# Performance work log

Measured on AMD Instinct MI355X. Metric: run time of the kernel, lower is better.

The kernel has to match this reference:

```python
import jax, jax.numpy as jnp
import numpy as np

N_PTS0 = 32   # sample points per line
N_PTS1 = 8    # after maxpool1d (kernel/stride = 4)
DIM_LOI = 128
DIM_FC = 1024
TOPK = 300
HW = 128
NLINES = 20000
NLAB = 3


def setup_inputs() -> dict:
    key = jax.random.key(0)
    ks = jax.random.split(key, 10)
    jloc = jax.random.uniform(ks[0], (1, HW, HW), dtype=jnp.float32)
    joff = jax.random.uniform(ks[1], (2, HW, HW), dtype=jnp.float32)
    loi_features = jax.random.normal(ks[2], (DIM_LOI, HW, HW), dtype=jnp.float32)
    edge_idx = jax.random.randint(ks[3], (NLINES, 2), 0, TOPK, dtype=jnp.int32)
    W1 = jax.random.normal(ks[4], (DIM_LOI * N_PTS1, DIM_FC), dtype=jnp.float32) * 0.02
    b1 = jnp.zeros((DIM_FC,), jnp.float32)
    W2 = jax.random.normal(ks[5], (DIM_FC, DIM_FC), dtype=jnp.float32) * 0.02
    b2 = jnp.zeros((DIM_FC,), jnp.float32)
    W3 = jax.random.normal(ks[6], (DIM_FC, NLAB), dtype=jnp.float32) * 0.02
    b3 = jnp.zeros((NLAB,), jnp.float32)
    return {"jloc": jloc, "joff": joff, "loi_features": loi_features,
            "edge_idx": edge_idx, "W1": W1, "b1": b1, "W2": W2, "b2": b2,
            "W3": W3, "b3": b3}


def reference(jloc, joff, loi_features, edge_idx, W1, b1, W2, b2, W3, b3):
    C, h, w = loi_features.shape
    # --- NMS: 3x3 max_pool2d, keep only local maxima ---
    ap = jax.lax.reduce_window(jloc, -jnp.inf, jax.lax.max,
                               (1, 3, 3), (1, 1, 1), 'SAME')
    jloc_nms = jloc * (jloc == ap).astype(jloc.dtype)
    # --- top-k junction decoding (joff_pred = sigmoid(joff) - 0.5) ---
    joff_pred = jax.nn.sigmoid(joff) - 0.5
    scores, idx = jax.lax.top_k(jloc_nms.reshape(-1), TOPK)
    joff_flat = joff_pred.reshape(2, -1)
    y = (idx // w).astype(jnp.float32) + joff_flat[1][idx] + 0.5
    x = (idx % w).astype(jnp.float32) + joff_flat[0][idx] + 0.5
    juncs = jnp.stack((x, y), axis=1)                       # [K, 2]
    # --- lines from junction pairs (lines_adjusted) ---
    lines = jnp.concatenate((juncs[edge_idx[:, 0]], juncs[edge_idx[:, 1]]), axis=1)  # [N, 4]
    # --- LOI pooling: bilinear sampling along each line ---
    tspan = jnp.linspace(0.0, 1.0, N_PTS0)                  # [P]
    U, V = lines[:, :2], lines[:, 2:]
    pts = U[:, :, None] * tspan + V[:, :, None] * (1.0 - tspan) - 0.5  # [N, 2, P]
    pts = pts.transpose(0, 2, 1).reshape(-1, 2)             # [N*P, 2]
    px, py = pts[:, 0], pts[:, 1]
    px0 = jnp.clip(jnp.floor(px), 0, w - 1)
    py0 = jnp.clip(jnp.floor(py), 0, h - 1)
    px1 = jnp.clip(px0 + 1, 0, w - 1)
    py1 = jnp.clip(py0 + 1, 0, h - 1)
    px0l, py0l = px0.astype(jnp.int32), py0.astype(jnp.int32)
    px1l, py1l = px1.astype(jnp.int32), py1.astype(jnp.int32)
    xp = (loi_features[:, py0l, px0l] * (py1 - py) * (px1 - px)
          + loi_features[:, py1l, px0l] * (py - py0) * (px1 - px)
          + loi_features[:, py0l, px1l] * (py1 - py) * (px - px0)
          + loi_features[:, py1l, px1l] * (py - py0) * (px - px0))  # [C, N*P]
    xp = xp.reshape(C, -1, N_PTS0).transpose(1, 0, 2)        # [N, C, P]
    k = N_PTS0 // N_PTS1
    xp = xp.reshape(xp.shape[0], C, N_PTS1, k).max(axis=-1)  # maxpool1d
    feats = xp.reshape(xp.shape[0], C * N_PTS1)              # [N, C*n_pts1]
    # --- fc2 MLP head ---
    h1 = jax.nn.relu(feats @ W1 + b1)
    h2 = jax.nn.relu(h1 @ W2 + b2)
    line_logits = h2 @ W3 + b3
    return line_logits
```

## Files before the change

### kernel.cpp

```cpp
#include <hip/hip_runtime.h>
#include <cmath>


typedef _Float16 f16;
typedef _Float16 f16x2 __attribute__((ext_vector_type(2)));
typedef _Float16 f16x8 __attribute__((ext_vector_type(8)));
typedef float f32x4 __attribute__((ext_vector_type(4)));

#define HWD 128
#define NPIX 16384
#define TOPK_N 300
#define NLINES 20000
#define MPAD 20160
#define KDIM 1024
#define NDIM 1024
#define MAXCAND 4096


#define G2L(gp, lp) __builtin_amdgcn_global_load_lds( \
    (const __attribute__((address_space(1))) void*)(gp), \
    (__attribute__((address_space(3))) void*)(lp), 16, 0, 0)

__global__ __launch_bounds__(256) void preproc_kernel(
    const float* __restrict__ loi, f16* __restrict__ loiT,
    const float* __restrict__ W1, f16* __restrict__ W1T,
    const float* __restrict__ W2, f16* __restrict__ W2T,
    const float* __restrict__ jloc, unsigned long long* __restrict__ cand,
    int* __restrict__ count, float* __restrict__ out, int out_n)
{
    const int bid = blockIdx.x;
    const int tid = threadIdx.x;
    if (bid < 128) {
        __shared__ f16 t[128 * 130];
        const int y = bid;
        #pragma unroll 4
        for (int it = 0; it < 64; ++it) {
            int idx = it * 256 + tid;
            int c = idx >> 7, x = idx & 127;
            t[x * 130 + c] = (f16)loi[c * NPIX + y * HWD + x];
        }
        __syncthreads();
        #pragma unroll
        for (int it = 0; it < 8; ++it) {
            int j = it * 256 + tid;
            int x = j >> 4, cc = (j & 15) * 8;
            f16x8 v;
            #pragma unroll
            for (int u = 0; u < 8; ++u) v[u] = t[x * 130 + cc + u];
            *(f16x8*)(loiT + (y * HWD + x) * HWD + cc) = v;
        }
    } else if (bid < 640) {
        const int b = bid - 128;
        const float* W = (b < 256) ? W1 : W2;
        f16* Wt = (b < 256) ? W1T : W2T;
        const int bb = b & 255;
        __shared__ f16 t[64 * 66];
        const int k0 = (bb >> 4) * 64;
        const int n0 = (bb & 15) * 64;
        #pragma unroll 4
        for (int it = 0; it < 16; ++it) {
            int i = it * 256 + tid;
            int r = i >> 6, c = i & 63;
            t[c * 66 + r] = (f16)W[(size_t)(k0 + r) * NDIM + n0 + c];
        }
        __syncthreads();
        #pragma unroll
        for (int it = 0; it < 2; ++it) {
            int j = it * 256 + tid;
            int nr = j >> 3, kc = (j & 7) * 8;
            f16x8 v;
            #pragma unroll
            for (int u = 0; u < 8; ++u) v[u] = t[nr * 66 + kc + u];
            const int kk = k0 + kc;
            const int n = n0 + nr;
            const int slot = ((kk >> 3) & 3) ^ ((n >> 1) & 3);
            *(f16x8*)(Wt + ((size_t)(kk >> 5) * NDIM + n) * 32 + slot * 8) = v;
        }
    } else if (bid < 704) {
        const int p = (bid - 640) * 256 + tid;
        const int y = p >> 7, x = p & 127;
        const float c = jloc[p];
        float m = c;
        for (int dy = -1; dy <= 1; ++dy) {
            int yy = y + dy;
            if (yy < 0 || yy >= HWD) continue;
            for (int dx = -1; dx <= 1; ++dx) {
                int xx = x + dx;
                if (xx < 0 || xx >= HWD) continue;
                m = fmaxf(m, jloc[yy * HWD + xx]);
            }
        }
        if (c == m && c > 0.0f) {
            int pos = atomicAdd(count, 1);
            if (pos < MAXCAND) {
                unsigned int ub = __float_as_uint(c);
                cand[pos] = ((unsigned long long)ub << 32) |
                            (unsigned long long)(0xFFFFFFFFu - (unsigned int)p);
            }
        }
    } else {
        const int base = (bid - 704) * 1024 + tid * 4;
        #pragma unroll
        for (int u = 0; u < 4; ++u)
            if (base + u < out_n) out[base + u] = 0.f;
    }
}

__global__ __launch_bounds__(256) void rank_junc_kernel(
    const unsigned long long* __restrict__ cand, const int* __restrict__ count,
    const float* __restrict__ joff, float* __restrict__ juncs )
{
    __shared__ unsigned long long keys[MAXCAND];
    const int n = min(*count, MAXCAND);
    const int t = blockIdx.x * 256 + threadIdx.x;
    for (int i = threadIdx.x; i < n; i += 256)
        keys[i] = cand[i];
    __syncthreads();
    if (t >= n) return;
    const unsigned long long key = keys[t];
    int rank = 0;
    int j = 0;
    for (; j + 4 <= n; j += 4) {
        rank += (keys[j]     > key);
        rank += (keys[j + 1] > key);
        rank += (keys[j + 2] > key);
        rank += (keys[j + 3] > key);
    }
    for (; j < n; ++j) rank += (keys[j] > key);
    if (rank < TOPK_N) {
        unsigned int p = 0xFFFFFFFFu - (unsigned int)(key & 0xFFFFFFFFull);
        float sx = 1.0f / (1.0f + expf(-joff[p]));
        float sy = 1.0f / (1.0f + expf(-joff[NPIX + p]));
        juncs[2 * rank + 0] = (float)(p & 127) + sx;
        juncs[2 * rank + 1] = (float)(p >> 7) + sy;
    }
}

__global__ __launch_bounds__(256) void sample_kernel(
    const f16* __restrict__ loiT, const float* __restrict__ juncs,
    const int* __restrict__ edge_idx, f16* __restrict__ feats)
{
    const int wv = threadIdx.x >> 6;
    const int l = blockIdx.x * 4 + wv;
    const int lane = threadIdx.x & 63;

    __shared__ int   soff[4][32][4];
    __shared__ float swt[4][32][4];

    if (lane < 32) {
        const int e0 = edge_idx[2 * l], e1 = edge_idx[2 * l + 1];
        const float ux = juncs[2 * e0], uy = juncs[2 * e0 + 1];
        const float vx = juncs[2 * e1], vy = juncs[2 * e1 + 1];
        const int j = lane;
        const float t = (float)j * (1.0f / 31.0f);
        const float px = ux * t + vx * (1.0f - t) - 0.5f;
        const float py = uy * t + vy * (1.0f - t) - 0.5f;
        float fx0 = fminf(fmaxf(floorf(px), 0.0f), 127.0f);
        float fy0 = fminf(fmaxf(floorf(py), 0.0f), 127.0f);
        float fx1 = fminf(fx0 + 1.0f, 127.0f);
        float fy1 = fminf(fy0 + 1.0f, 127.0f);
        int ix0 = (int)fx0, iy0 = (int)fy0, ix1 = (int)fx1, iy1 = (int)fy1;
        soff[wv][j][0] = (iy0 * HWD + ix0) * HWD;
        soff[wv][j][1] = (iy1 * HWD + ix0) * HWD;
        soff[wv][j][2] = (iy0 * HWD + ix1) * HWD;
        soff[wv][j][3] = (iy1 * HWD + ix1) * HWD;
        swt[wv][j][0] = (fy1 - py) * (fx1 - px);
        swt[wv][j][1] = (py - fy0) * (fx1 - px);
        swt[wv][j][2] = (fy1 - py) * (px - fx0);
        swt[wv][j][3] = (py - fy0) * (px - fx0);
    }
    __syncthreads();

    const int c2 = lane * 2;
    f16x8 o0, o1;
    #pragma unroll
    for (int p = 0; p < 8; ++p) {
        float m0 = -INFINITY, m1 = -INFINITY;
        #pragma unroll
        for (int jj = 0; jj < 4; ++jj) {
            const int j = p * 4 + jj;
            const int b00 = soff[wv][j][0], b10 = soff[wv][j][1];
            const int b01 = soff[wv][j][2], b11 = soff[wv][j][3];
            const float w00 = swt[wv][j][0], w10 = swt[wv][j][1];
            const float w01 = swt[wv][j][2], w11 = swt[wv][j][3];
            f16x2 v00 = *(const f16x2*)(loiT + b00 + c2);
            f16x2 v10 = *(const f16x2*)(loiT + b10 + c2);
            f16x2 v01 = *(const f16x2*)(loiT + b01 + c2);
            f16x2 v11 = *(const f16x2*)(loiT + b11 + c2);
            float s0 = (float)v00.x * w00 + (float)v10.x * w10 +
                       (float)v01.x * w01 + (float)v11.x * w11;
            float s1 = (float)v00.y * w00 + (float)v10.y * w10 +
                       (float)v01.y * w01 + (float)v11.y * w11;
            m0 = fmaxf(m0, s0);
            m1 = fmaxf(m1, s1);
        }
        o0[p] = (f16)m0;
        o1[p] = (f16)m1;
    }
    const int rs = (l >> 1) & 3;
    const int oct0 = (lane & 1) * 2;
    f16* base = feats + ((size_t)(lane >> 1) * MPAD + l) * 32;
    *(f16x8*)(base + ((oct0 ^ rs) * 8)) = o0;
    *(f16x8*)(base + (((oct0 + 1) ^ rs) * 8)) = o1;
}

__global__ __launch_bounds__(256, 2) void gemm_bias_relu_kernel(
    const f16* __restrict__ A, const f16* __restrict__ Bt,
    const float* __restrict__ bias, f16* __restrict__ C,
    const float* __restrict__ W3, const float* __restrict__ b3,
    float* __restrict__ out, int K, int head)
{
    extern __shared__ f16 lds[];
    const int tid = threadIdx.x;
    const int wave = tid >> 6, lane = tid & 63;
    const int wm = wave >> 1, wn = wave & 1;
    const int m0 = blockIdx.y * 160;
    const int n0 = blockIdx.x * 256;

    const int col16 = lane & 15;
    const int quad = lane >> 4;
    const int swz = (quad ^ ((col16 >> 1) & 3)) * 8;

    f32x4 acc[5][8];
    #pragma unroll
    for (int mi = 0; mi < 5; ++mi)
        #pragma unroll
        for (int ni = 0; ni < 8; ++ni)
            acc[mi][ni] = (f32x4){0.f, 0.f, 0.f, 0.f};

    const size_t strideA = (size_t)MPAD * 32;
    const size_t strideB = (size_t)NDIM * 32;
    const f16* gA = A + (size_t)m0 * 32 + wave * 512 + lane * 8;
    const f16* gB = Bt + (size_t)n0 * 32 + wave * 2048 + lane * 8;
    const int sAo = wave * 512;
    const int sBo = wave * 2048;

#define STAGE(CN) do { \
        f16* lb_ = lds + ((CN) % 3) * 13312; \
        const f16* ga_ = gA + (size_t)(CN) * strideA; \
        G2L(ga_,        lb_ + sAo); \
        G2L(ga_ + 2048, lb_ + sAo + 2048); \
        if (wave < 2) G2L(ga_ + 4096, lb_ + sAo + 4096); \
        const f16* gb_ = gB + (size_t)(CN) * strideB; \
        G2L(gb_,        lb_ + 5120 + sBo); \
        G2L(gb_ + 512,  lb_ + 5120 + sBo + 512); \
        G2L(gb_ + 1024, lb_ + 5120 + sBo + 1024); \
        G2L(gb_ + 1536, lb_ + 5120 + sBo + 1536); \
    } while (0)

    STAGE(0);
    asm volatile("" ::: "memory");
    STAGE(1);
    asm volatile("" ::: "memory");

    const int NC = K >> 5;
    for (int c = 0; c < NC; ++c) {
        if (c + 1 < NC) {
            if (wave < 2) asm volatile("s_waitcnt vmcnt(7)" ::: "memory");
            else          asm volatile("s_waitcnt vmcnt(6)" ::: "memory");
        } else {
            asm volatile("s_waitcnt vmcnt(0)" ::: "memory");
        }
        __builtin_amdgcn_s_barrier();
        if (c + 2 < NC) STAGE(c + 2);
        asm volatile("" ::: "memory");

        const f16* buf = lds + (c % 3) * 13312;
        const f16* pA = buf + (wm * 80 + col16) * 32 + swz;
        const f16* pB = buf + 5120 + (wn * 128 + col16) * 32 + swz;
        f16x8 af[5], bf[8];
        #pragma unroll
        for (int i = 0; i < 5; ++i)
            af[i] = *(const f16x8*)(pA + i * 512);
        #pragma unroll
        for (int i = 0; i < 8; ++i)
            bf[i] = *(const f16x8*)(pB + i * 512);
        #pragma unroll
        for (int mi = 0; mi < 5; ++mi)
            #pragma unroll
            for (int ni = 0; ni < 8; ++ni)
                acc[mi][ni] = __builtin_amdgcn_mfma_f32_16x16x32_f16(
                    af[mi], bf[ni], acc[mi][ni], 0, 0, 0);
    }
#undef STAGE

    if (!head) {
        #pragma unroll
        for (int ni = 0; ni < 8; ++ni) {
            const int n = n0 + wn * 128 + ni * 16 + col16;
            const float b = bias[n];
            const size_t rb = (size_t)(n >> 5) * MPAD;
            const int noct = (n >> 3) & 3, ne = n & 7;
            #pragma unroll
            for (int mi = 0; mi < 5; ++mi) {
                #pragma unroll
                for (int r = 0; r < 4; ++r) {
                    const int m = m0 + wm * 80 + mi * 16 + quad * 4 + r;
                    float v = fmaxf(acc[mi][ni][r] + b, 0.f);
                    C[(rb + m) * 32 + ((noct ^ ((m >> 1) & 3)) * 8) + ne] = (f16)v;
                }
            }
        }
    } else {
        float bb[8], w3c[8][3];
        #pragma unroll
        for (int ni = 0; ni < 8; ++ni) {
            const int n = n0 + wn * 128 + ni * 16 + col16;
            bb[ni] = bias[n];
            #pragma unroll
            for (int jj = 0; jj < 3; ++jj) w3c[ni][jj] = W3[n * 3 + jj];
        }
        const bool addb3 = (blockIdx.x == 0 && wn == 0);
        #pragma unroll
        for (int mi = 0; mi < 5; ++mi) {
            #pragma unroll
            for (int r = 0; r < 4; ++r) {
                float s0 = 0.f, s1 = 0.f, s2 = 0.f;
                #pragma unroll
                for (int ni = 0; ni < 8; ++ni) {
                    float v = fmaxf(acc[mi][ni][r] + bb[ni], 0.f);
                    s0 += v * w3c[ni][0];
                    s1 += v * w3c[ni][1];
                    s2 += v * w3c[ni][2];
                }
                #pragma unroll
                for (int mask = 1; mask <= 8; mask <<= 1) {
                    s0 += __shfl_xor(s0, mask);
                    s1 += __shfl_xor(s1, mask);
                    s2 += __shfl_xor(s2, mask);
                }
                if (col16 == 0) {
                    const int m = m0 + wm * 80 + mi * 16 + quad * 4 + r;
                    if (m < NLINES) {
                        atomicAdd(&out[m * 3 + 0], s0 + (addb3 ? b3[0] : 0.f));
                        atomicAdd(&out[m * 3 + 1], s1 + (addb3 ? b3[1] : 0.f));
                        atomicAdd(&out[m * 3 + 2], s2 + (addb3 ? b3[2] : 0.f));
                    }
                }
            }
        }
    }
}

extern "C" void kernel_launch(void* const* d_in, const int* in_sizes, int n_in,
                              void* d_out, int out_size, void* d_ws, size_t ws_size,
                              hipStream_t stream)
{
    const float* jloc = (const float*)d_in[0];
    const float* joff = (const float*)d_in[1];
    const float* loi  = (const float*)d_in[2];
    const int*   eidx = (const int*)d_in[3];
    const float* W1   = (const float*)d_in[4];
    const float* b1   = (const float*)d_in[5];
    const float* W2   = (const float*)d_in[6];
    const float* b2   = (const float*)d_in[7];
    const float* W3   = (const float*)d_in[8];
    const float* b3   = (const float*)d_in[9];
    float* out = (float*)d_out;

    char* ws = (char*)d_ws;
    f16*   loiT  = (f16*)(ws);
    f16*   W1T   = (f16*)(ws + ((size_t)4 << 20));
    f16*   W2T   = (f16*)(ws + ((size_t)6 << 20));
    float* juncs = (float*)(ws + ((size_t)8 << 20));
    int*   count = (int*)(ws + ((size_t)8 << 20) + 4096);
    unsigned long long* cand =
        (unsigned long long*)(ws + ((size_t)8 << 20) + 8192);
    f16*   feats = (f16*)(ws + ((size_t)9 << 20));
    f16*   h1    = (f16*)(ws + ((size_t)52 << 20));

    static int attr_done = 0;
    if (!attr_done) {
        (void)hipFuncSetAttribute(
            reinterpret_cast<const void*>(&gemm_bias_relu_kernel),
            hipFuncAttributeMaxDynamicSharedMemorySize, 79872);
        attr_done = 1;
    }

    hipMemsetAsync(count, 0, sizeof(int), stream);
    preproc_kernel<<<dim3(764), dim3(256), 0, stream>>>(
        loi, loiT, W1, W1T, W2, W2T, jloc, cand, count, out, out_size);
    rank_junc_kernel<<<dim3(MAXCAND / 256), dim3(256), 0, stream>>>(
        cand, count, joff, juncs);
    sample_kernel<<<dim3(NLINES / 4), dim3(256), 0, stream>>>(loiT, juncs, eidx, feats);
    gemm_bias_relu_kernel<<<dim3(NDIM / 256, MPAD / 160), dim3(256), 79872, stream>>>(
        feats, W1T, b1, h1, nullptr, nullptr, nullptr, KDIM, 0);
    gemm_bias_relu_kernel<<<dim3(NDIM / 256, MPAD / 160), dim3(256), 79872, stream>>>(
        h1, W2T, b2, nullptr, W3, b3, out, KDIM, 1);
}
```

Measured before the change: 277.8 us.

## Double GEMM K-step per stage to 64 with larger LDS ring buffers

Each pipeline stage of the GEMM now loads two 32-wide K chunks per barrier, so each LDS buffer holds 64 of K and the triple-buffered ring grows to about 156 KB. The aim is to halve the number of barriers and waitcnt synchronisation points and keep more loads in flight. In exchange, occupancy drops to one block per CU (launch bounds changed from 2 to 1), so there is less latency hiding across blocks.

```diff
diff --git a/kernel.cpp b/kernel.cpp
--- a/kernel.cpp
+++ b/kernel.cpp
@@ -204,7 +204,7 @@
     *(f16x8*)(base + (((oct0 + 1) ^ rs) * 8)) = o1;
 }
 
-__global__ __launch_bounds__(256, 2) void gemm_bias_relu_kernel(
+__global__ __launch_bounds__(256, 1) void gemm_bias_relu_kernel(
     const f16* __restrict__ A, const f16* __restrict__ Bt,
     const float* __restrict__ bias, f16* __restrict__ C,
     const float* __restrict__ W3, const float* __restrict__ b3,
@@ -230,22 +230,26 @@
 
     const size_t strideA = (size_t)MPAD * 32;
     const size_t strideB = (size_t)NDIM * 32;
-    const f16* gA = A + (size_t)m0 * 32 + wave * 512 + lane * 8;
-    const f16* gB = Bt + (size_t)n0 * 32 + wave * 2048 + lane * 8;
-    const int sAo = wave * 512;
-    const int sBo = wave * 2048;
-
-#define STAGE(CN) do { \
-        f16* lb_ = lds + ((CN) % 3) * 13312; \
-        const f16* ga_ = gA + (size_t)(CN) * strideA; \
-        G2L(ga_,        lb_ + sAo); \
-        G2L(ga_ + 2048, lb_ + sAo + 2048); \
-        if (wave < 2) G2L(ga_ + 4096, lb_ + sAo + 4096); \
-        const f16* gb_ = gB + (size_t)(CN) * strideB; \
-        G2L(gb_,        lb_ + 5120 + sBo); \
-        G2L(gb_ + 512,  lb_ + 5120 + sBo + 512); \
-        G2L(gb_ + 1024, lb_ + 5120 + sBo + 1024); \
-        G2L(gb_ + 1536, lb_ + 5120 + sBo + 1536); \
+    const f16* gA = A + (size_t)m0 * 32 + lane * 8;
+    const f16* gB = Bt + (size_t)n0 * 32 + lane * 8;
+
+#define STAGE(R) do { \
+        f16* lb_ = lds + ((R) % 3) * 26624; \
+        const f16* gar_ = gA + (size_t)(2 * (R)) * strideA; \
+        _Pragma("unroll") \
+        for (int i_ = 0; i_ < 5; ++i_) { \
+            const int s_ = wave + 4 * i_; \
+            const f16* g_ = gar_ + (s_ >= 10 ? strideA : 0) + (s_ % 10) * 512; \
+            G2L(g_, lb_ + s_ * 512); \
+        } \
+        const f16* gbr_ = gB + (size_t)(2 * (R)) * strideB \
+                          + (wave >= 2 ? strideB : 0); \
+        const int sb0_ = 8 * wave; \
+        _Pragma("unroll") \
+        for (int j_ = 0; j_ < 8; ++j_) { \
+            const int sB_ = sb0_ + j_; \
+            G2L(gbr_ + (sB_ & 15) * 512, lb_ + 10240 + sB_ * 512); \
+        } \
     } while (0)
 
     STAGE(0);
@@ -253,34 +257,51 @@
     STAGE(1);
     asm volatile("" ::: "memory");
 
-    const int NC = K >> 5;
-    for (int c = 0; c < NC; ++c) {
-        if (c + 1 < NC) {
-            if (wave < 2) asm volatile("s_waitcnt vmcnt(7)" ::: "memory");
-            else          asm volatile("s_waitcnt vmcnt(6)" ::: "memory");
-        } else {
+    const int NR = K >> 6;
+    for (int r = 0; r < NR; ++r) {
+        if (r + 1 < NR)
+            asm volatile("s_waitcnt vmcnt(13)" ::: "memory");
+        else
             asm volatile("s_waitcnt vmcnt(0)" ::: "memory");
-        }
         __builtin_amdgcn_s_barrier();
-        if (c + 2 < NC) STAGE(c + 2);
+        if (r + 2 < NR) STAGE(r + 2);
         asm volatile("" ::: "memory");
 
-        const f16* buf = lds + (c % 3) * 13312;
-        const f16* pA = buf + (wm * 80 + col16) * 32 + swz;
-        const f16* pB = buf + 5120 + (wn * 128 + col16) * 32 + swz;
-        f16x8 af[5], bf[8];
-        #pragma unroll
-        for (int i = 0; i < 5; ++i)
-            af[i] = *(const f16x8*)(pA + i * 512);
-        #pragma unroll
-        for (int i = 0; i < 8; ++i)
-            bf[i] = *(const f16x8*)(pB + i * 512);
-        #pragma unroll
-        for (int mi = 0; mi < 5; ++mi)
-            #pragma unroll
-            for (int ni = 0; ni < 8; ++ni)
-                acc[mi][ni] = __builtin_amdgcn_mfma_f32_16x16x32_f16(
-                    af[mi], bf[ni], acc[mi][ni], 0, 0, 0);
+        const f16* buf = lds + (r % 3) * 26624;
+        {
+            const f16* pA = buf + (wm * 80 + col16) * 32 + swz;
+            const f16* pB = buf + 10240 + (wn * 128 + col16) * 32 + swz;
+            f16x8 af[5], bf[8];
+            #pragma unroll
+            for (int i = 0; i < 5; ++i)
+                af[i] = *(const f16x8*)(pA + i * 512);
+            #pragma unroll
+            for (int i = 0; i < 8; ++i)
+                bf[i] = *(const f16x8*)(pB + i * 512);
+            #pragma unroll
+            for (int mi = 0; mi < 5; ++mi)
+                #pragma unroll
+                for (int ni = 0; ni < 8; ++ni)
+                    acc[mi][ni] = __builtin_amdgcn_mfma_f32_16x16x32_f16(
+                        af[mi], bf[ni], acc[mi][ni], 0, 0, 0);
+        }
+        {
+            const f16* pA = buf + 5120 + (wm * 80 + col16) * 32 + swz;
+            const f16* pB = buf + 18432 + (wn * 128 + col16) * 32 + swz;
+            f16x8 af[5], bf[8];
+            #pragma unroll
+            for (int i = 0; i < 5; ++i)
+                af[i] = *(const f16x8*)(pA + i * 512);
+            #pragma unroll
+            for (int i = 0; i < 8; ++i)
+                bf[i] = *(const f16x8*)(pB + i * 512);
+            #pragma unroll
+            for (int mi = 0; mi < 5; ++mi)
+                #pragma unroll
+                for (int ni = 0; ni < 8; ++ni)
+                    acc[mi][ni] = __builtin_amdgcn_mfma_f32_16x16x32_f16(
+                        af[mi], bf[ni], acc[mi][ni], 0, 0, 0);
+        }
     }
 #undef STAGE
 
@@ -373,7 +394,7 @@
     if (!attr_done) {
         (void)hipFuncSetAttribute(
             reinterpret_cast<const void*>(&gemm_bias_relu_kernel),
-            hipFuncAttributeMaxDynamicSharedMemorySize, 79872);
+            hipFuncAttributeMaxDynamicSharedMemorySize, 159744);
         attr_done = 1;
     }
 
@@ -383,8 +404,8 @@
     rank_junc_kernel<<<dim3(MAXCAND / 256), dim3(256), 0, stream>>>(
         cand, count, joff, juncs);
     sample_kernel<<<dim3(NLINES / 4), dim3(256), 0, stream>>>(loiT, juncs, eidx, feats);
-    gemm_bias_relu_kernel<<<dim3(NDIM / 256, MPAD / 160), dim3(256), 79872, stream>>>(
+    gemm_bias_relu_kernel<<<dim3(NDIM / 256, MPAD / 160), dim3(256), 159744, stream>>>(
         feats, W1T, b1, h1, nullptr, nullptr, nullptr, KDIM, 0);
-    gemm_bias_relu_kernel<<<dim3(NDIM / 256, MPAD / 160), dim3(256), 79872, stream>>>(
+    gemm_bias_relu_kernel<<<dim3(NDIM / 256, MPAD / 160), dim3(256), 159744, stream>>>(
         h1, W2T, b2, nullptr, W3, b3, out, KDIM, 1);
 }
```

Result: slower. 291.8 us (+5.0%).
